# Kernel tuning notes

Hardware: AMD Instinct MI355X
Metric: run time of the kernel (lower is better)

The kernel has to match this reference:

```python
import jax, jax.numpy as jnp
import numpy as np

EMBED_DIM = 768
FF_DIM = 3072
NUM_EXPERTS = 8
TOP_K = 2
CAPACITY_FACTOR = 1.25  # training-mode capacity factor
LB_WEIGHT = 0.01
Z_WEIGHT = 0.001


def setup_inputs() -> dict:
    key = jax.random.key(0)
    k0, k1, k2, k3, k4 = jax.random.split(key, 5)
    B, S, D, F, E = 4, 2048, EMBED_DIM, FF_DIM, NUM_EXPERTS
    scale_d = 1.0 / np.sqrt(D)
    scale_f = 1.0 / np.sqrt(F)
    return {
        "x": jax.random.normal(k0, (B, S, D), dtype=jnp.float32),
        # router gate: nn.Linear(D, E, bias=False) -> weight [E, D]
        "w_gate": jax.random.normal(k1, (E, D), dtype=jnp.float32) * scale_d,
        # stacked expert weights, torch Linear layout [out, in]
        "wi_gate": jax.random.normal(k2, (E, F, D), dtype=jnp.float32) * scale_d,
        "wi_up": jax.random.normal(k3, (E, F, D), dtype=jnp.float32) * scale_d,
        "wo": jax.random.normal(k4, (E, D, F), dtype=jnp.float32) * scale_f,
    }


def moe_forward(x, w_gate, wi_gate, wi_up, wo):
    B, S, D = x.shape
    E = w_gate.shape[0]
    K = TOP_K
    T = B * S
    capacity = max(int(T * K / E * CAPACITY_FACTOR), K)

    xf = x.reshape(T, D)
    router_logits = xf @ w_gate.T                        # [T, E]
    router_probs = jax.nn.softmax(router_logits, axis=-1)
    topk_probs, topk_idx = jax.lax.top_k(router_probs, K)  # [T, K]
    topk_probs = topk_probs / topk_probs.sum(axis=-1, keepdims=True)

    # one-hot dispatch mask [T, K, E]
    onehot = (topk_idx[:, :, None] == jnp.arange(E)[None, None, :]).astype(xf.dtype)
    # per-(k, expert) arrival rank of each token (torch truncates first `capacity`
    # tokens in token-index order, independently per k and per expert)
    rank = ((jnp.cumsum(onehot, axis=0) - onehot) * onehot).sum(-1)  # [T, K]
    keep = (rank < capacity).astype(xf.dtype)                        # [T, K]

    # combine weights per (token, expert) [T, E]
    combine = jnp.einsum('tk,tk,tke->te', topk_probs, keep, onehot)

    out = jnp.zeros_like(xf)
    for e in range(E):  # fixed small structural loop over experts
        gate = jax.nn.silu(xf @ wi_gate[e].T)   # [T, F]
        up = xf @ wi_up[e].T                    # [T, F]
        y = (gate * up) @ wo[e].T               # [T, D]
        out = out + y * combine[:, e:e + 1]

    # auxiliary losses
    expert_mask = onehot.sum(axis=1)            # [T, E]
    f = expert_mask.sum(axis=0) / (T * K)
    P = router_probs.mean(axis=0)
    load_balance_loss = E * (f * P).sum()
    z_loss = jnp.mean(jax.nn.logsumexp(router_logits, axis=-1) ** 2)
    aux_loss = LB_WEIGHT * load_balance_loss + Z_WEIGHT * z_loss

    return out.reshape(B, S, D), aux_loss


def reference(x, w_gate, wi_gate, wi_up, wo):
    return moe_forward(x, w_gate, wi_gate, wi_up, wo)
```

## Files before the change

### kernel.cpp

```cpp
#include <hip/hip_runtime.h>

typedef unsigned short u16;
typedef unsigned int u32;
typedef unsigned long long u64;

#define T_TOK 8192
#define DIM 768
#define FF 3072
#define NE 8
#define CAP 2560
#define LSTR 5120
#define MAXMT 20

typedef __attribute__((ext_vector_type(8))) short s8v;
typedef __attribute__((ext_vector_type(4))) float f4v;

__device__ __forceinline__ u16 f2bf(float f) {
  union { float f; u32 u; } v; v.f = f;
  u32 r = v.u + 0x7FFFu + ((v.u >> 16) & 1u);
  return (u16)(r >> 16);
}

__device__ __forceinline__ void glds16(const void* g, void* l) {
  __builtin_amdgcn_global_load_lds(
      (const __attribute__((address_space(1))) u32*)g,
      (__attribute__((address_space(3))) u32*)l, 16, 0, 0);
}

__global__ void cast_bf16_kernel(const float* __restrict__ src, u16* __restrict__ dst, int n8) {
  int i = blockIdx.x * blockDim.x + threadIdx.x;
  if (i >= n8) return;
  const float4* s4 = (const float4*)src;
  float4 a = s4[2 * i], b = s4[2 * i + 1];
  uint4 o;
  o.x = (u32)f2bf(a.x) | ((u32)f2bf(a.y) << 16);
  o.y = (u32)f2bf(a.z) | ((u32)f2bf(a.w) << 16);
  o.z = (u32)f2bf(b.x) | ((u32)f2bf(b.y) << 16);
  o.w = (u32)f2bf(b.z) | ((u32)f2bf(b.w) << 16);
  ((uint4*)dst)[i] = o;
}

__global__ __launch_bounds__(256) void router_kernel(
    const float* __restrict__ x, const float* __restrict__ wg,
    int* __restrict__ tki, float* __restrict__ tkp,
    float* __restrict__ probs, float* __restrict__ lse2) {
  int lane = threadIdx.x & 63;
  int t = blockIdx.x * 4 + (threadIdx.x >> 6);
  const float* xr = x + (long)t * DIM;
  float acc[NE];
#pragma unroll
  for (int e = 0; e < NE; e++) acc[e] = 0.f;
  for (int i = 0; i < DIM / 64; i++) {
    float xv = xr[lane + 64 * i];
#pragma unroll
    for (int e = 0; e < NE; e++) acc[e] += xv * wg[e * DIM + lane + 64 * i];
  }
#pragma unroll
  for (int off = 32; off > 0; off >>= 1) {
#pragma unroll
    for (int e = 0; e < NE; e++) acc[e] += __shfl_xor(acc[e], off);
  }
  if (lane == 0) {
    float m = acc[0];
#pragma unroll
    for (int e = 1; e < NE; e++) m = fmaxf(m, acc[e]);
    float p[NE], s = 0.f;
#pragma unroll
    for (int e = 0; e < NE; e++) { p[e] = __expf(acc[e] - m); s += p[e]; }
    float inv = 1.f / s;
    int e0 = 0;
#pragma unroll
    for (int e = 1; e < NE; e++) if (acc[e] > acc[e0]) e0 = e;
    int e1 = (e0 == 0) ? 1 : 0;
#pragma unroll
    for (int e = 0; e < NE; e++) if (e != e0 && acc[e] > acc[e1]) e1 = e;
    float p0 = p[e0] * inv, p1 = p[e1] * inv;
    float rn = 1.f / (p0 + p1);
    tki[2 * t] = e0; tki[2 * t + 1] = e1;
    tkp[2 * t] = p0 * rn; tkp[2 * t + 1] = p1 * rn;
    float4 pa = {p[0] * inv, p[1] * inv, p[2] * inv, p[3] * inv};
    float4 pb = {p[4] * inv, p[5] * inv, p[6] * inv, p[7] * inv};
    ((float4*)(probs + t * 8))[0] = pa;
    ((float4*)(probs + t * 8))[1] = pb;
    float lse = __logf(s) + m;
    lse2[t] = lse * lse;
  }
}

__global__ __launch_bounds__(1024) void reduce_router_kernel(
    const int* __restrict__ tki, const float* __restrict__ probs, const float* __restrict__ lse2,
    int* __restrict__ fcnt, float* __restrict__ psum, float* __restrict__ zsum) {
  int t = blockIdx.x * 1024 + threadIdx.x;
  float4 pa = ((const float4*)(probs + t * 8))[0];
  float4 pb = ((const float4*)(probs + t * 8))[1];
  float p[8] = {pa.x, pa.y, pa.z, pa.w, pb.x, pb.y, pb.z, pb.w};
  float z = lse2[t];
  int e0 = tki[2 * t], e1 = tki[2 * t + 1];
  int fc[8];
#pragma unroll
  for (int e = 0; e < 8; e++) fc[e] = (e0 == e ? 1 : 0) + (e1 == e ? 1 : 0);
#pragma unroll
  for (int off = 32; off > 0; off >>= 1) {
#pragma unroll
    for (int e = 0; e < 8; e++) { p[e] += __shfl_xor(p[e], off); fc[e] += __shfl_xor(fc[e], off); }
    z += __shfl_xor(z, off);
  }
  __shared__ float sp[16][9];
  __shared__ int sf[16][8];
  int wv = threadIdx.x >> 6, lane = threadIdx.x & 63;
  if (lane == 0) {
#pragma unroll
    for (int e = 0; e < 8; e++) { sp[wv][e] = p[e]; sf[wv][e] = fc[e]; }
    sp[wv][8] = z;
  }
  __syncthreads();
  if (threadIdx.x < 9) {
    float s = 0.f;
    for (int w = 0; w < 16; w++) s += sp[w][threadIdx.x];
    if (threadIdx.x < 8) atomicAdd(&psum[threadIdx.x], s);
    else atomicAdd(zsum, s);
  }
  if (threadIdx.x >= 64 && threadIdx.x < 72) {
    int e = threadIdx.x - 64;
    int s = 0;
    for (int w = 0; w < 16; w++) s += sf[w][e];
    atomicAdd(&fcnt[e], s);
  }
}

__global__ __launch_bounds__(1024) void rank_dispatch_kernel(
    const int* __restrict__ tki, const float* __restrict__ tkp,
    int* __restrict__ ltk, float* __restrict__ lw,
    int* __restrict__ counts, int* __restrict__ baserow) {
  __shared__ int wave_cnt[2][16][8];
  __shared__ int base[2][8];
  __shared__ int epos[8];
  int tid = threadIdx.x, wv = tid >> 6, lane = tid & 63;
  if (tid < 16) base[tid >> 3][tid & 7] = 0;
  if (tid < 8) epos[tid] = 0;
  __syncthreads();
  u64 lmask = (lane == 63) ? 0x7FFFFFFFFFFFFFFFull : ((1ull << lane) - 1ull);
  for (int c = 0; c < T_TOK / 1024; c++) {
    int t = c * 1024 + tid;
    int e0 = tki[2 * t], e1 = tki[2 * t + 1];
    float p0 = tkp[2 * t], p1 = tkp[2 * t + 1];
    int pre0 = 0, pre1 = 0;
    for (int e = 0; e < 8; e++) {
      u64 m0 = __ballot(e0 == e);
      if (e0 == e) pre0 = __popcll(m0 & lmask);
      if (lane == 0) wave_cnt[0][wv][e] = __popcll(m0);
      u64 m1 = __ballot(e1 == e);
      if (e1 == e) pre1 = __popcll(m1 & lmask);
      if (lane == 0) wave_cnt[1][wv][e] = __popcll(m1);
    }
    __syncthreads();
    if (tid < 16) {
      int k = tid >> 3, e = tid & 7;
      int run = base[k][e];
      for (int w = 0; w < 16; w++) {
        int v = wave_cnt[k][w][e];
        wave_cnt[k][w][e] = run;
        run += v;
      }
      base[k][e] = run;
    }
    __syncthreads();
    int r0 = wave_cnt[0][wv][e0] + pre0;
    int r1 = wave_cnt[1][wv][e1] + pre1;
    if (r0 < CAP) { int p = atomicAdd(&epos[e0], 1); ltk[e0 * LSTR + p] = (t << 1); lw[e0 * LSTR + p] = p0; }
    if (r1 < CAP) { int p = atomicAdd(&epos[e1], 1); ltk[e1 * LSTR + p] = (t << 1) | 1; lw[e1 * LSTR + p] = p1; }
    __syncthreads();
  }
  if (tid == 0) {
    int run = 0;
    for (int e = 0; e < 8; e++) { counts[e] = epos[e]; baserow[e] = run; run += epos[e]; }
  }
}

__global__ __launch_bounds__(256, 2) void gemm1_kernel(
    const u16* __restrict__ xb, const u16* __restrict__ wgb, const u16* __restrict__ wub,
    u16* __restrict__ H, const int* __restrict__ counts, const int* __restrict__ baserow,
    const int* __restrict__ ltk) {
  int id = blockIdx.x;
  int xcd = id & 7;
  int q = id >> 3;
  int gg = q / MAXMT;
  int mt = q - gg * MAXMT;
  int g = gg * 8 + xcd;
  int e = g / 48;
  int nt = g - e * 48;
  int cnt = counts[e];
  if (mt * 128 >= cnt) return;

  __shared__ u16 As[128 * 32];
  __shared__ u16 Bg[64 * 32];
  __shared__ u16 Bu[64 * 32];
  __shared__ int toks[128];
  int tid = threadIdx.x;
  if (tid < 128) {
    int r = mt * 128 + tid; if (r > cnt - 1) r = cnt - 1;
    toks[tid] = ltk[e * LSTR + r] >> 1;
  }
  __syncthreads();
  int rq = tid >> 2;
  int kc = (tid & 3) * 8;
  long tA0 = toks[rq], tA1 = toks[64 + rq];
  const u16* gA0 = xb + tA0 * DIM + kc;
  const u16* gA1 = xb + tA1 * DIM + kc;
  long bOff = ((long)e * FF + nt * 64 + rq) * DIM + kc;
  const u16* gG0 = wgb + bOff;
  const u16* gU0 = wub + bOff;
  u16* dA0 = As + tid * 8; u16* dA1 = As + (256 + tid) * 8;
  u16* dG0 = Bg + tid * 8;
  u16* dU0 = Bu + tid * 8;

  int lane = tid & 63, wv = tid >> 6;
  int wm = (wv & 1) * 64, wn = (wv >> 1) * 32;
  int lrow = lane & 15, quad = lane >> 4;

  f4v zero = {0.f, 0.f, 0.f, 0.f};
  f4v accg[4][2], accu[4][2];
#pragma unroll
  for (int i = 0; i < 4; i++)
#pragma unroll
    for (int j = 0; j < 2; j++) { accg[i][j] = zero; accu[i][j] = zero; }

  for (int kt = 0; kt < DIM / 32; kt++) {
    int ko = kt * 32;
    __syncthreads();
    glds16(gA0 + ko, dA0); glds16(gA1 + ko, dA1);
    glds16(gG0 + ko, dG0);
    glds16(gU0 + ko, dU0);
    __syncthreads();
    s8v a[4], bg[2], bu[2];
#pragma unroll
    for (int i = 0; i < 4; i++)
      a[i] = *(const s8v*)&As[(wm + i * 16 + lrow) * 32 + quad * 8];
#pragma unroll
    for (int j = 0; j < 2; j++) {
      bg[j] = *(const s8v*)&Bg[(wn + j * 16 + lrow) * 32 + quad * 8];
      bu[j] = *(const s8v*)&Bu[(wn + j * 16 + lrow) * 32 + quad * 8];
    }
#pragma unroll
    for (int i = 0; i < 4; i++)
#pragma unroll
      for (int j = 0; j < 2; j++) {
        accg[i][j] = __builtin_amdgcn_mfma_f32_16x16x32_bf16(a[i], bg[j], accg[i][j], 0, 0, 0);
        accu[i][j] = __builtin_amdgcn_mfma_f32_16x16x32_bf16(a[i], bu[j], accu[i][j], 0, 0, 0);
      }
  }
  long hb = (long)baserow[e] + (long)mt * 128;
#pragma unroll
  for (int i = 0; i < 4; i++) {
#pragma unroll
    for (int r = 0; r < 4; r++) {
      int m = wm + i * 16 + quad * 4 + r;
      if (mt * 128 + m < cnt) {
#pragma unroll
        for (int j = 0; j < 2; j++) {
          float gv = accg[i][j][r], uv = accu[i][j][r];
          float h = gv / (1.f + __expf(-gv)) * uv;
          H[(hb + m) * FF + nt * 64 + wn + j * 16 + lrow] = f2bf(h);
        }
      }
    }
  }
}

__global__ __launch_bounds__(256, 2) void gemm2_kernel(
    const u16* __restrict__ H, const u16* __restrict__ wob,
    float* __restrict__ out, const int* __restrict__ counts, const int* __restrict__ baserow,
    const int* __restrict__ ltk, const float* __restrict__ lw) {
  int id = blockIdx.x;
  int xcd = id & 7;
  int q = id >> 3;
  int gg = q / 6;
  int nt = q - gg * 6;
  int g = gg * 8 + xcd;
  int e = g / MAXMT;
  int mt = g - e * MAXMT;
  int cnt = counts[e];
  if (mt * 128 >= cnt) return;

  __shared__ u16 As[128 * 32];
  __shared__ u16 Bs[128 * 32];
  __shared__ int stok[128];
  __shared__ float sw[128];
  int tid = threadIdx.x;
  if (tid < 128) {
    int r = mt * 128 + tid; if (r > cnt - 1) r = cnt - 1;
    stok[tid] = ltk[e * LSTR + r];
    sw[tid] = lw[e * LSTR + r];
  }
  long hb = (long)baserow[e] + (long)mt * 128;
  int rq = tid >> 2, kc = (tid & 3) * 8;
  const u16* gA0 = H + (hb + rq) * FF + kc;
  const u16* gA1 = gA0 + 64l * FF;
  long bOff = ((long)e * DIM + nt * 128 + rq) * FF + kc;
  const u16* gB0 = wob + bOff;
  const u16* gB1 = gB0 + 64l * FF;
  u16* dA0 = As + tid * 8; u16* dA1 = As + (256 + tid) * 8;
  u16* dB0 = Bs + tid * 8; u16* dB1 = Bs + (256 + tid) * 8;
  int lane = tid & 63, wv = tid >> 6;
  int wm = (wv & 1) * 64, wn = (wv >> 1) * 64;
  int lrow = lane & 15, quad = lane >> 4;
  f4v zero = {0.f, 0.f, 0.f, 0.f};
  f4v acc[4][4];
#pragma unroll
  for (int i = 0; i < 4; i++)
#pragma unroll
    for (int j = 0; j < 4; j++) acc[i][j] = zero;

  for (int kt = 0; kt < FF / 32; kt++) {
    int ko = kt * 32;
    __syncthreads();
    glds16(gA0 + ko, dA0); glds16(gA1 + ko, dA1);
    glds16(gB0 + ko, dB0); glds16(gB1 + ko, dB1);
    __syncthreads();
    s8v a[4], b[4];
#pragma unroll
    for (int i = 0; i < 4; i++)
      a[i] = *(const s8v*)&As[(wm + i * 16 + lrow) * 32 + quad * 8];
#pragma unroll
    for (int j = 0; j < 4; j++)
      b[j] = *(const s8v*)&Bs[(wn + j * 16 + lrow) * 32 + quad * 8];
#pragma unroll
    for (int i = 0; i < 4; i++)
#pragma unroll
      for (int j = 0; j < 4; j++)
        acc[i][j] = __builtin_amdgcn_mfma_f32_16x16x32_bf16(a[i], b[j], acc[i][j], 0, 0, 0);
  }
#pragma unroll
  for (int i = 0; i < 4; i++) {
#pragma unroll
    for (int r = 0; r < 4; r++) {
      int m = wm + i * 16 + quad * 4 + r;
      if (mt * 128 + m < cnt) {
        int entry = stok[m];
        int t = entry >> 1;
        float w = sw[m];
        long ob = (long)t * DIM + nt * 128;
#pragma unroll
        for (int j = 0; j < 4; j++)
          atomicAdd(&out[ob + wn + j * 16 + lrow], acc[i][j][r] * w);
      }
    }
  }
}

__global__ void aux_kernel(const int* __restrict__ fcnt, const float* __restrict__ psum,
                           const float* __restrict__ zsum, float* __restrict__ outaux) {
  if (threadIdx.x == 0 && blockIdx.x == 0) {
    float lb = 0.f;
    for (int e = 0; e < 8; e++)
      lb += ((float)fcnt[e] / (float)(T_TOK * 2)) * (psum[e] / (float)T_TOK);
    lb *= 8.f;
    float z = zsum[0] / (float)T_TOK;
    outaux[0] = 0.01f * lb + 0.001f * z;
  }
}

extern "C" void kernel_launch(void* const* d_in, const int* in_sizes, int n_in,
                              void* d_out, int out_size, void* d_ws, size_t ws_size,
                              hipStream_t stream) {
  const float* x = (const float*)d_in[0];
  const float* wgate = (const float*)d_in[1];
  const float* wig = (const float*)d_in[2];
  const float* wiu = (const float*)d_in[3];
  const float* wo = (const float*)d_in[4];
  float* out = (float*)d_out;

  char* ws = (char*)d_ws;
  size_t off = 0;
  auto alloc = [&](size_t bytes) {
    void* p = ws + off;
    off += (bytes + 255) & ~(size_t)255;
    return p;
  };
  int* ctrl = (int*)alloc(256);
  u16* xb = (u16*)alloc((size_t)T_TOK * DIM * 2);
  u16* wgb = (u16*)alloc((size_t)NE * FF * DIM * 2);
  u16* wub = (u16*)alloc((size_t)NE * FF * DIM * 2);
  u16* wob = (u16*)alloc((size_t)NE * DIM * FF * 2);
  u16* Hbuf = (u16*)alloc((size_t)(T_TOK * 2 + 128) * FF * 2);
  int* tki = (int*)alloc((size_t)T_TOK * 2 * 4);
  float* tkp = (float*)alloc((size_t)T_TOK * 2 * 4);
  int* ltk = (int*)alloc((size_t)NE * LSTR * 4);
  float* lw = (float*)alloc((size_t)NE * LSTR * 4);
  float* probs = (float*)alloc((size_t)T_TOK * 8 * 4);
  float* lse2 = (float*)alloc((size_t)T_TOK * 4);

  int* fcnt = ctrl;
  int* counts = ctrl + 8;
  int* baserow = ctrl + 16;
  float* psum = (float*)(ctrl + 24);
  float* zsum = (float*)(ctrl + 32);

  hipMemsetAsync(ctrl, 0, 256, stream);
  hipMemsetAsync(out, 0, (size_t)out_size * 4, stream);
  cast_bf16_kernel<<<T_TOK * DIM / 8 / 256, 256, 0, stream>>>(x, xb, T_TOK * DIM / 8);
  cast_bf16_kernel<<<NE * FF * DIM / 8 / 256, 256, 0, stream>>>(wig, wgb, NE * FF * DIM / 8);
  cast_bf16_kernel<<<NE * FF * DIM / 8 / 256, 256, 0, stream>>>(wiu, wub, NE * FF * DIM / 8);
  cast_bf16_kernel<<<NE * DIM * FF / 8 / 256, 256, 0, stream>>>(wo, wob, NE * DIM * FF / 8);
  router_kernel<<<T_TOK / 4, 256, 0, stream>>>(x, wgate, tki, tkp, probs, lse2);
  reduce_router_kernel<<<T_TOK / 1024, 1024, 0, stream>>>(tki, probs, lse2, fcnt, psum, zsum);
  rank_dispatch_kernel<<<1, 1024, 0, stream>>>(tki, tkp, ltk, lw, counts, baserow);
  gemm1_kernel<<<8 * 48 * MAXMT, 256, 0, stream>>>(xb, wgb, wub, Hbuf, counts, baserow, ltk);
  gemm2_kernel<<<8 * MAXMT * 6, 256, 0, stream>>>(Hbuf, wob, out, counts, baserow, ltk, lw);
  aux_kernel<<<1, 64, 0, stream>>>(fcnt, psum, zsum, out + (size_t)T_TOK * DIM);
}
```

Baseline: 641.7 us.

## Load GEMM weight fragments directly to registers with prefetch; fuse weight casts

Both expert GEMMs now read weight (B) fragments straight from global memory into registers in MFMA operand layout, prefetching the next k-step while the current one computes, instead of staging them in LDS. The A tile is still staged through LDS but in a layout that each wave reads contiguously. The three weight cast launches are merged into one launch with a 3-slice grid. This cuts LDS traffic and launch count. In exchange, the uncoalesced 16-byte-per-lane global loads of weights add register pressure and are not shared across waves.

```diff
diff --git a/kernel.cpp b/kernel.cpp
--- a/kernel.cpp
+++ b/kernel.cpp
@@ -30,6 +30,23 @@
 __global__ void cast_bf16_kernel(const float* __restrict__ src, u16* __restrict__ dst, int n8) {
   int i = blockIdx.x * blockDim.x + threadIdx.x;
   if (i >= n8) return;
+  const float4* s4 = (const float4*)src;
+  float4 a = s4[2 * i], b = s4[2 * i + 1];
+  uint4 o;
+  o.x = (u32)f2bf(a.x) | ((u32)f2bf(a.y) << 16);
+  o.y = (u32)f2bf(a.z) | ((u32)f2bf(a.w) << 16);
+  o.z = (u32)f2bf(b.x) | ((u32)f2bf(b.y) << 16);
+  o.w = (u32)f2bf(b.z) | ((u32)f2bf(b.w) << 16);
+  ((uint4*)dst)[i] = o;
+}
+
+__global__ void cast3_bf16_kernel(const float* __restrict__ s0, const float* __restrict__ s1,
+                                  const float* __restrict__ s2, u16* __restrict__ d0,
+                                  u16* __restrict__ d1, u16* __restrict__ d2, int n8) {
+  int i = blockIdx.x * blockDim.x + threadIdx.x;
+  if (i >= n8) return;
+  const float* src = (blockIdx.y == 0) ? s0 : (blockIdx.y == 1) ? s1 : s2;
+  u16* dst = (blockIdx.y == 0) ? d0 : (blockIdx.y == 1) ? d1 : d2;
   const float4* s4 = (const float4*)src;
   float4 a = s4[2 * i], b = s4[2 * i + 1];
   uint4 o;
@@ -193,8 +210,6 @@
   if (mt * 128 >= cnt) return;
 
   __shared__ u16 As[128 * 32];
-  __shared__ u16 Bg[64 * 32];
-  __shared__ u16 Bu[64 * 32];
   __shared__ int toks[128];
   int tid = threadIdx.x;
   if (tid < 128) {
@@ -202,21 +217,25 @@
     toks[tid] = ltk[e * LSTR + r] >> 1;
   }
   __syncthreads();
-  int rq = tid >> 2;
-  int kc = (tid & 3) * 8;
-  long tA0 = toks[rq], tA1 = toks[64 + rq];
-  const u16* gA0 = xb + tA0 * DIM + kc;
-  const u16* gA1 = xb + tA1 * DIM + kc;
-  long bOff = ((long)e * FF + nt * 64 + rq) * DIM + kc;
-  const u16* gG0 = wgb + bOff;
-  const u16* gU0 = wub + bOff;
-  u16* dA0 = As + tid * 8; u16* dA1 = As + (256 + tid) * 8;
-  u16* dG0 = Bg + tid * 8;
-  u16* dU0 = Bu + tid * 8;
 
   int lane = tid & 63, wv = tid >> 6;
+  int sr = lane & 15, sq = lane >> 4;
+  long t0 = toks[wv * 16 + sr];
+  long t1 = toks[64 + wv * 16 + sr];
+  const u16* gA0 = xb + t0 * DIM + sq * 8;
+  const u16* gA1 = xb + t1 * DIM + sq * 8;
+  u16* dA0 = As + (size_t)tid * 8;
+  u16* dA1 = As + (size_t)(256 + tid) * 8;
+
   int wm = (wv & 1) * 64, wn = (wv >> 1) * 32;
-  int lrow = lane & 15, quad = lane >> 4;
+  int lrow = sr, quad = sq;
+  int agbase = (wv & 1) * 4;
+
+  long bRow = (long)e * FF + nt * 64 + wn + sr;
+  const u16* pG0 = wgb + bRow * DIM + sq * 8;
+  const u16* pG1 = pG0 + 16l * DIM;
+  const u16* pU0 = wub + bRow * DIM + sq * 8;
+  const u16* pU1 = pU0 + 16l * DIM;
 
   f4v zero = {0.f, 0.f, 0.f, 0.f};
   f4v accg[4][2], accu[4][2];
@@ -225,29 +244,35 @@
 #pragma unroll
     for (int j = 0; j < 2; j++) { accg[i][j] = zero; accu[i][j] = zero; }
 
+  s8v cg0 = *(const s8v*)(pG0);
+  s8v cg1 = *(const s8v*)(pG1);
+  s8v cu0 = *(const s8v*)(pU0);
+  s8v cu1 = *(const s8v*)(pU1);
+
+#pragma unroll 2
   for (int kt = 0; kt < DIM / 32; kt++) {
     int ko = kt * 32;
     __syncthreads();
-    glds16(gA0 + ko, dA0); glds16(gA1 + ko, dA1);
-    glds16(gG0 + ko, dG0);
-    glds16(gU0 + ko, dU0);
-    __syncthreads();
-    s8v a[4], bg[2], bu[2];
+    glds16(gA0 + ko, dA0);
+    glds16(gA1 + ko, dA1);
+    int k2 = (ko + 32 < DIM) ? (ko + 32) : ko;
+    s8v ng0 = *(const s8v*)(pG0 + k2);
+    s8v ng1 = *(const s8v*)(pG1 + k2);
+    s8v nu0 = *(const s8v*)(pU0 + k2);
+    s8v nu1 = *(const s8v*)(pU1 + k2);
+    __syncthreads();
+    s8v a[4];
 #pragma unroll
     for (int i = 0; i < 4; i++)
-      a[i] = *(const s8v*)&As[(wm + i * 16 + lrow) * 32 + quad * 8];
-#pragma unroll
-    for (int j = 0; j < 2; j++) {
-      bg[j] = *(const s8v*)&Bg[(wn + j * 16 + lrow) * 32 + quad * 8];
-      bu[j] = *(const s8v*)&Bu[(wn + j * 16 + lrow) * 32 + quad * 8];
-    }
-#pragma unroll
-    for (int i = 0; i < 4; i++)
-#pragma unroll
-      for (int j = 0; j < 2; j++) {
-        accg[i][j] = __builtin_amdgcn_mfma_f32_16x16x32_bf16(a[i], bg[j], accg[i][j], 0, 0, 0);
-        accu[i][j] = __builtin_amdgcn_mfma_f32_16x16x32_bf16(a[i], bu[j], accu[i][j], 0, 0, 0);
-      }
+      a[i] = *(const s8v*)&As[(agbase + i) * 512 + lane * 8];
+#pragma unroll
+    for (int i = 0; i < 4; i++) {
+      accg[i][0] = __builtin_amdgcn_mfma_f32_16x16x32_bf16(a[i], cg0, accg[i][0], 0, 0, 0);
+      accg[i][1] = __builtin_amdgcn_mfma_f32_16x16x32_bf16(a[i], cg1, accg[i][1], 0, 0, 0);
+      accu[i][0] = __builtin_amdgcn_mfma_f32_16x16x32_bf16(a[i], cu0, accu[i][0], 0, 0, 0);
+      accu[i][1] = __builtin_amdgcn_mfma_f32_16x16x32_bf16(a[i], cu1, accu[i][1], 0, 0, 0);
+    }
+    cg0 = ng0; cg1 = ng1; cu0 = nu0; cu1 = nu1;
   }
   long hb = (long)baserow[e] + (long)mt * 128;
 #pragma unroll
@@ -283,7 +308,6 @@
   if (mt * 128 >= cnt) return;
 
   __shared__ u16 As[128 * 32];
-  __shared__ u16 Bs[128 * 32];
   __shared__ int stok[128];
   __shared__ float sw[128];
   int tid = threadIdx.x;
@@ -292,18 +316,25 @@
     stok[tid] = ltk[e * LSTR + r];
     sw[tid] = lw[e * LSTR + r];
   }
+  __syncthreads();
   long hb = (long)baserow[e] + (long)mt * 128;
-  int rq = tid >> 2, kc = (tid & 3) * 8;
-  const u16* gA0 = H + (hb + rq) * FF + kc;
-  const u16* gA1 = gA0 + 64l * FF;
-  long bOff = ((long)e * DIM + nt * 128 + rq) * FF + kc;
-  const u16* gB0 = wob + bOff;
-  const u16* gB1 = gB0 + 64l * FF;
-  u16* dA0 = As + tid * 8; u16* dA1 = As + (256 + tid) * 8;
-  u16* dB0 = Bs + tid * 8; u16* dB1 = Bs + (256 + tid) * 8;
   int lane = tid & 63, wv = tid >> 6;
+  int sr = lane & 15, sq = lane >> 4;
+  const u16* gA0 = H + (hb + wv * 16 + sr) * FF + sq * 8;
+  const u16* gA1 = H + (hb + 64 + wv * 16 + sr) * FF + sq * 8;
+  u16* dA0 = As + (size_t)tid * 8;
+  u16* dA1 = As + (size_t)(256 + tid) * 8;
+
   int wm = (wv & 1) * 64, wn = (wv >> 1) * 64;
-  int lrow = lane & 15, quad = lane >> 4;
+  int lrow = sr, quad = sq;
+  int agbase = (wv & 1) * 4;
+
+  long bRow = (long)e * DIM + nt * 128 + wn + sr;
+  const u16* pB0 = wob + bRow * FF + sq * 8;
+  const u16* pB1 = pB0 + 16l * FF;
+  const u16* pB2 = pB0 + 32l * FF;
+  const u16* pB3 = pB0 + 48l * FF;
+
   f4v zero = {0.f, 0.f, 0.f, 0.f};
   f4v acc[4][4];
 #pragma unroll
@@ -311,24 +342,35 @@
 #pragma unroll
     for (int j = 0; j < 4; j++) acc[i][j] = zero;
 
+  s8v cb0 = *(const s8v*)(pB0);
+  s8v cb1 = *(const s8v*)(pB1);
+  s8v cb2 = *(const s8v*)(pB2);
+  s8v cb3 = *(const s8v*)(pB3);
+
+#pragma unroll 2
   for (int kt = 0; kt < FF / 32; kt++) {
     int ko = kt * 32;
     __syncthreads();
-    glds16(gA0 + ko, dA0); glds16(gA1 + ko, dA1);
-    glds16(gB0 + ko, dB0); glds16(gB1 + ko, dB1);
-    __syncthreads();
-    s8v a[4], b[4];
+    glds16(gA0 + ko, dA0);
+    glds16(gA1 + ko, dA1);
+    int k2 = (ko + 32 < FF) ? (ko + 32) : ko;
+    s8v nb0 = *(const s8v*)(pB0 + k2);
+    s8v nb1 = *(const s8v*)(pB1 + k2);
+    s8v nb2 = *(const s8v*)(pB2 + k2);
+    s8v nb3 = *(const s8v*)(pB3 + k2);
+    __syncthreads();
+    s8v a[4];
 #pragma unroll
     for (int i = 0; i < 4; i++)
-      a[i] = *(const s8v*)&As[(wm + i * 16 + lrow) * 32 + quad * 8];
-#pragma unroll
-    for (int j = 0; j < 4; j++)
-      b[j] = *(const s8v*)&Bs[(wn + j * 16 + lrow) * 32 + quad * 8];
-#pragma unroll
-    for (int i = 0; i < 4; i++)
-#pragma unroll
-      for (int j = 0; j < 4; j++)
-        acc[i][j] = __builtin_amdgcn_mfma_f32_16x16x32_bf16(a[i], b[j], acc[i][j], 0, 0, 0);
+      a[i] = *(const s8v*)&As[(agbase + i) * 512 + lane * 8];
+#pragma unroll
+    for (int i = 0; i < 4; i++) {
+      acc[i][0] = __builtin_amdgcn_mfma_f32_16x16x32_bf16(a[i], cb0, acc[i][0], 0, 0, 0);
+      acc[i][1] = __builtin_amdgcn_mfma_f32_16x16x32_bf16(a[i], cb1, acc[i][1], 0, 0, 0);
+      acc[i][2] = __builtin_amdgcn_mfma_f32_16x16x32_bf16(a[i], cb2, acc[i][2], 0, 0, 0);
+      acc[i][3] = __builtin_amdgcn_mfma_f32_16x16x32_bf16(a[i], cb3, acc[i][3], 0, 0, 0);
+    }
+    cb0 = nb0; cb1 = nb1; cb2 = nb2; cb3 = nb3;
   }
 #pragma unroll
   for (int i = 0; i < 4; i++) {
@@ -399,9 +441,8 @@
   hipMemsetAsync(ctrl, 0, 256, stream);
   hipMemsetAsync(out, 0, (size_t)out_size * 4, stream);
   cast_bf16_kernel<<<T_TOK * DIM / 8 / 256, 256, 0, stream>>>(x, xb, T_TOK * DIM / 8);
-  cast_bf16_kernel<<<NE * FF * DIM / 8 / 256, 256, 0, stream>>>(wig, wgb, NE * FF * DIM / 8);
-  cast_bf16_kernel<<<NE * FF * DIM / 8 / 256, 256, 0, stream>>>(wiu, wub, NE * FF * DIM / 8);
-  cast_bf16_kernel<<<NE * DIM * FF / 8 / 256, 256, 0, stream>>>(wo, wob, NE * DIM * FF / 8);
+  cast3_bf16_kernel<<<dim3(NE * FF * DIM / 8 / 256, 3), 256, 0, stream>>>(
+      wig, wiu, wo, wgb, wub, wob, NE * FF * DIM / 8);
   router_kernel<<<T_TOK / 4, 256, 0, stream>>>(x, wgate, tki, tkp, probs, lse2);
   reduce_router_kernel<<<T_TOK / 1024, 1024, 0, stream>>>(tki, probs, lse2, fcnt, psum, zsum);
   rank_dispatch_kernel<<<1, 1024, 0, stream>>>(tki, tkp, ltk, lw, counts, baserow);
```

Measured after the change: 1.055 ms. 64.4% more time.
